# Kernel optimization log

Measured on AMD Instinct MI355X. Metric: run time of the kernel, lower is better.

The kernel has to match this reference:

```python
import jax, jax.numpy as jnp
import numpy as np

B, S, D = 4, 2048, 1024      # batch, seq, d_model
H = 4096                     # expert hidden_size
E, K = 8, 2                  # num_experts, top_k
Z_COEF, BAL_COEF = 0.001, 0.01


def setup_inputs() -> dict:
    key = jax.random.key(0)
    ks = jax.random.split(key, 10)
    sc = 0.02
    return {
        "x": jax.random.normal(ks[0], (B, S, D), jnp.float32),
        "gate_w": jax.random.normal(ks[1], (D, E), jnp.float32) * sc,
        "keys_w": jax.random.normal(ks[2], (E, D, H), jnp.float32) * sc,
        "keys_b": jnp.zeros((E, H), jnp.float32),
        "values_w": jax.random.normal(ks[3], (E, H, D), jnp.float32) * sc,
        "values_b": jnp.zeros((E, D), jnp.float32),
        "shared_keys_w": jax.random.normal(ks[4], (D, H), jnp.float32) * sc,
        "shared_keys_b": jnp.zeros((H,), jnp.float32),
        "shared_values_w": jax.random.normal(ks[5], (H, D), jnp.float32) * sc,
        "shared_values_b": jnp.zeros((D,), jnp.float32),
    }


def reference(x, gate_w, keys_w, keys_b, values_w, values_b,
              shared_keys_w, shared_keys_b, shared_values_w, shared_values_b):
    b, s, d = x.shape
    xf = x.reshape(-1, d)                                  # [N, D]

    # ---- Router (top-k, softmax over selected scores) ----
    logits = xf @ gate_w                                   # [N, E]
    scores, idx = jax.lax.top_k(logits, K)                 # [N, K]
    w = jax.nn.softmax(scores, axis=-1)                    # [N, K]

    # Aux losses (training path)
    one_hot = jax.nn.one_hot(idx, E, dtype=w.dtype)        # [N, K, E]
    usage = (one_hot * w[..., None]).sum(axis=(0, 1))      # [E]
    balance_loss = usage.std() / usage.mean() * BAL_COEF
    z_loss = jnp.square(jax.nn.logsumexp(logits, axis=-1)).mean() * Z_COEF
    router_loss = balance_loss + z_loss

    # ---- Shared expert(s): single FFN, divided by count (=1) ----
    out = jax.nn.gelu(xf @ shared_keys_w + shared_keys_b) @ shared_values_w + shared_values_b

    # ---- Training path: dense per-expert FFN, masked combine ----
    # hidden: [N, E, H]
    hidden = jax.nn.gelu(jnp.einsum('nd,edh->neh', xf, keys_w) + keys_b)
    expert_out = jnp.einsum('neh,ehd->ned', hidden, values_w) + values_b  # [N, E, D]
    comb = (one_hot * w[..., None]).sum(axis=1)            # [N, E] per-token expert weight
    out = out + jnp.einsum('ned,ne->nd', expert_out, comb)

    return out.reshape(b, s, d), router_loss
```

## Files before the change

kernel.cpp:

```cpp
#include <hip/hip_runtime.h>
#include <hip/hip_bf16.h>


#define N_TOK 8192
#define DM    1024
#define HD    4096
#define NE    8
#define NKTOT 16384
#define PERM_CAP 17408
#define MAX_TILES 136
#define BAND 17
#define EV_BLOCKS 1088
#define RTOK_BLK 16

typedef __attribute__((ext_vector_type(8))) short bhalf8;
typedef __attribute__((ext_vector_type(8))) unsigned short ushort8v;
typedef __attribute__((ext_vector_type(4))) float floatx4;

__device__ __forceinline__ unsigned short f2bf(float f) {
  union { float f; unsigned int u; } v; v.f = f;
  unsigned int u = v.u;
  return (unsigned short)((u + 0x7fffu + ((u >> 16) & 1u)) >> 16);
}

__device__ __forceinline__ float bf2f(unsigned short h) {
  union { unsigned int u; float f; } v; v.u = ((unsigned int)h) << 16;
  return v.f;
}

__device__ __forceinline__ float gelu_tanh(float h) {
  float u = 0.7978845608028654f * (h + 0.044715f * h * h * h);
  float t = 1.0f - 2.0f / (1.0f + __expf(2.0f * u));
  return 0.5f * h * (1.0f + t);
}

__device__ __forceinline__ void gload16(const unsigned short* g, void* l) {
  __builtin_amdgcn_global_load_lds(
      (const __attribute__((address_space(1))) void*)g,
      (__attribute__((address_space(3))) void*)l, 16, 0, 0);
}

__global__ void init_kernel(int* perm, float* permw, float* usage, float* zsum,
                            int* counts, int* fill) {
  int i = blockIdx.x * 256 + threadIdx.x;
  if (i < PERM_CAP) { perm[i] = 0; permw[i] = 0.0f; }
  if (i < NE) { usage[i] = 0.0f; counts[i] = 0; fill[i] = 0; }
  if (i == 0) zsum[0] = 0.0f;
}

__global__ void cvt_x_kernel(const float* __restrict__ x, unsigned short* __restrict__ xb) {
  size_t i = (size_t)(blockIdx.x * 256 + threadIdx.x) * 4;
  float4 v = *(const float4*)(x + i);
  ushort4 o;
  o.x = f2bf(v.x); o.y = f2bf(v.y); o.z = f2bf(v.z); o.w = f2bf(v.w);
  *(ushort4*)(xb + i) = o;
}

__global__ void router_kernel(const float* __restrict__ x, const float* __restrict__ gw,
                              int* __restrict__ idxb, float* __restrict__ wbuf,
                              float* __restrict__ usage, float* __restrict__ zsum,
                              int* __restrict__ counts) {
  __shared__ float s_use[NE];
  __shared__ int   s_cnt[NE];
  __shared__ float s_z;
  int t = threadIdx.x;
  if (t < NE) { s_use[t] = 0.0f; s_cnt[t] = 0; }
  if (t == 0) s_z = 0.0f;
  __syncthreads();

  int wave = t >> 6;
  int lane = t & 63;

  float luse[NE]; int lcnt[NE];
#pragma unroll
  for (int e = 0; e < NE; e++) { luse[e] = 0.0f; lcnt[e] = 0; }
  float lz = 0.0f;

#pragma unroll
  for (int i = 0; i < 4; i++) {
    int n = blockIdx.x * RTOK_BLK + wave * 4 + i;
    const float* xr = x + (size_t)n * DM;
    float acc[NE];
#pragma unroll
    for (int e = 0; e < NE; e++) acc[e] = 0.0f;
    for (int d = lane; d < DM; d += 64) {
      float xv = xr[d];
      const float* g = gw + (size_t)d * NE;
#pragma unroll
      for (int e = 0; e < NE; e++) acc[e] += xv * g[e];
    }
#pragma unroll
    for (int e = 0; e < NE; e++) {
#pragma unroll
      for (int off = 32; off > 0; off >>= 1) acc[e] += __shfl_xor(acc[e], off);
    }
    if (lane == 0) {
      float m1 = acc[0]; int i1 = 0;
#pragma unroll
      for (int e = 1; e < NE; e++) if (acc[e] > m1) { m1 = acc[e]; i1 = e; }
      float m2 = -3.0e38f; int i2 = 0;
#pragma unroll
      for (int e = 0; e < NE; e++) if (e != i1 && acc[e] > m2) { m2 = acc[e]; i2 = e; }
      float e1 = __expf(m2 - m1);
      float w1 = 1.0f / (1.0f + e1);
      float w2 = e1 / (1.0f + e1);
      float s = 0.0f;
#pragma unroll
      for (int e = 0; e < NE; e++) s += __expf(acc[e] - m1);
      float lse = m1 + __logf(s);
      idxb[n * 2 + 0] = i1; idxb[n * 2 + 1] = i2;
      wbuf[n * 2 + 0] = w1; wbuf[n * 2 + 1] = w2;
      luse[i1] += w1; luse[i2] += w2;
      lcnt[i1]++;     lcnt[i2]++;
      lz += lse * lse;
    }
  }

  if (lane == 0) {
#pragma unroll
    for (int e = 0; e < NE; e++) {
      atomicAdd(&s_use[e], luse[e]);
      atomicAdd(&s_cnt[e], lcnt[e]);
    }
    atomicAdd(&s_z, lz);
  }
  __syncthreads();
  if (t < NE) {
    atomicAdd(&usage[t], s_use[t]);
    atomicAdd(&counts[t], s_cnt[t]);
  }
  if (t == 0) atomicAdd(zsum, s_z);
}

__global__ void scan_kernel(const int* __restrict__ counts, int* __restrict__ poff,
                            int* __restrict__ tileE, int* __restrict__ tileR,
                            int* __restrict__ nTiles,
                            const float* __restrict__ usage, const float* __restrict__ zsum,
                            float* __restrict__ lossOut) {
  if (threadIdx.x == 0 && blockIdx.x == 0) {
    int run = 0, nt = 0;
    for (int e = 0; e < NE; e++) {
      poff[e] = run;
      int t = (counts[e] + 127) >> 7;
      for (int i = 0; i < t; i++) { tileE[nt] = e; tileR[nt] = run + i * 128; nt++; }
      run += t << 7;
    }
    *nTiles = nt;
    float mean = 0.0f;
    for (int e = 0; e < NE; e++) mean += usage[e];
    mean *= (1.0f / NE);
    float var = 0.0f;
    for (int e = 0; e < NE; e++) { float d = usage[e] - mean; var += d * d; }
    var *= (1.0f / NE);
    float bal = sqrtf(var) / mean * 0.01f;
    float z = (zsum[0] / (float)N_TOK) * 0.001f;
    lossOut[0] = bal + z;
  }
}

__global__ void scatter_kernel(const int* __restrict__ idxb, const float* __restrict__ wbuf,
                               const int* __restrict__ poff, int* __restrict__ fill,
                               int* __restrict__ perm, float* __restrict__ permw,
                               int* __restrict__ pos) {
  __shared__ int lcnt[NE];
  __shared__ int lbase[NE];
  int t = threadIdx.x;
  if (t < NE) lcnt[t] = 0;
  __syncthreads();
  int i = blockIdx.x * 256 + t;
  int e = idxb[i];
  int r = atomicAdd(&lcnt[e], 1);
  __syncthreads();
  if (t < NE) lbase[t] = atomicAdd(&fill[t], lcnt[t]);
  __syncthreads();
  int p = poff[e] + lbase[e] + r;
  perm[p] = i >> 1;
  permw[p] = wbuf[i];
  pos[i] = p;
}

__global__ void transpose_cvt_kernel(const float* __restrict__ src,
                                     unsigned short* __restrict__ dst, int R, int C) {
  __shared__ float tile[64][65];
  size_t bo = (size_t)blockIdx.z * R * C;
  src += bo; dst += bo;
  int r0 = blockIdx.x * 64, c0 = blockIdx.y * 64;
  int c = threadIdx.x & 63, r = threadIdx.x >> 6;
#pragma unroll
  for (int i = 0; i < 16; i++)
    tile[r + i * 4][c] = src[(size_t)(r0 + r + i * 4) * C + c0 + c];
  __syncthreads();
  int u = threadIdx.x & 7;
  int ow = threadIdx.x >> 3;
#pragma unroll
  for (int it = 0; it < 2; it++) {
    int oc = ow + it * 32;
    ushort8v o;
#pragma unroll
    for (int j = 0; j < 8; j++) o[j] = f2bf(tile[u * 8 + j][oc]);
    *(ushort8v*)&dst[(size_t)(c0 + oc) * R + r0 + u * 8] = o;
  }
}

__global__ void combine_kernel(float* __restrict__ out,
                               const unsigned short* __restrict__ eout,
                               const int* __restrict__ pos) {
  int t = blockIdx.x;
  int d = threadIdx.x * 8;
  int p0 = pos[t * 2], p1 = pos[t * 2 + 1];
  float* o = out + (size_t)t * DM + d;
  const unsigned short* e0 = eout + (size_t)p0 * DM + d;
  const unsigned short* e1 = eout + (size_t)p1 * DM + d;
  float4 a = *(const float4*)(o);
  float4 b = *(const float4*)(o + 4);
  ushort4 u0a = *(const ushort4*)(e0), u0b = *(const ushort4*)(e0 + 4);
  ushort4 u1a = *(const ushort4*)(e1), u1b = *(const ushort4*)(e1 + 4);
  a.x += bf2f(u0a.x) + bf2f(u1a.x);
  a.y += bf2f(u0a.y) + bf2f(u1a.y);
  a.z += bf2f(u0a.z) + bf2f(u1a.z);
  a.w += bf2f(u0a.w) + bf2f(u1a.w);
  b.x += bf2f(u0b.x) + bf2f(u1b.x);
  b.y += bf2f(u0b.y) + bf2f(u1b.y);
  b.z += bf2f(u0b.z) + bf2f(u1b.z);
  b.w += bf2f(u0b.w) + bf2f(u1b.w);
  *(float4*)(o) = a;
  *(float4*)(o + 4) = b;
}

template<int MODE>
__device__ __forceinline__ void gemm_body(
    int id,
    const unsigned short* __restrict__ A,
    const unsigned short* __restrict__ BT,
    const float* __restrict__ bias,
    float* __restrict__ outF,
    unsigned short* __restrict__ outH,
    int Kd, int Nd,
    const int* __restrict__ perm,
    const int* __restrict__ tileE,
    const int* __restrict__ tileR,
    const int* __restrict__ nTiles) {
  __shared__ __align__(16) unsigned short As[128 * 64];
  __shared__ __align__(16) unsigned short Bs[128 * 64];

  int xcd = id & 7, q = id >> 3;
  int mt, ntile;
  if (MODE == 1) {
    ntile = q & 7;
    mt = xcd * 8 + (q >> 3);
  } else {
    int n_in = q & 7, m_in = (q >> 3) & 3, ng = (q >> 5) & 3, mg = q >> 7;
    int mband = mg * 4 + m_in;
    if (mband >= BAND) return;
    mt = xcd * BAND + mband;
    ntile = ng * 8 + n_in;
  }

  int n0 = ntile * 128;
  int prow0 = 0, m0 = 0;
  if (MODE == 2) {
    if (mt >= *nTiles) return;
    int e = tileE[mt];
    prow0 = tileR[mt];
    BT += (size_t)e * Kd * Nd;
    bias += (size_t)e * Nd;
  } else {
    m0 = mt * 128;
  }

  int t = threadIdx.x;
  int rsub = t >> 3;
  int gc = (t & 7) ^ (rsub & 7);
  const unsigned short* aptr[4];
  const unsigned short* bptr[4];
#pragma unroll
  for (int p = 0; p < 4; p++) {
    int r = rsub + p * 32;
    size_t grow;
    if (MODE == 2) grow = (size_t)perm[prow0 + r];
    else           grow = (size_t)(m0 + r);
    aptr[p] = A + grow * Kd + gc * 8;
    bptr[p] = BT + (size_t)(n0 + r) * Kd + gc * 8;
  }
  char* ldsA = (char*)As + (t & 192) * 16;
  char* ldsB = (char*)Bs + (t & 192) * 16;

  int lane = t & 63;
  int wv = t >> 6;
  int wm = (wv >> 1) * 64, wn = (wv & 1) * 64;
  int lr = lane & 15, lq = lane >> 4;
  int rx = lr & 7;

  floatx4 acc[4][4];
#pragma unroll
  for (int i = 0; i < 4; i++)
#pragma unroll
    for (int j = 0; j < 4; j++) acc[i][j] = (floatx4){0.f, 0.f, 0.f, 0.f};

  for (int k0 = 0; k0 < Kd; k0 += 64) {
#pragma unroll
    for (int p = 0; p < 4; p++) {
      gload16(aptr[p] + k0, ldsA + p * 4096);
      gload16(bptr[p] + k0, ldsB + p * 4096);
    }
    __syncthreads();
#pragma unroll
    for (int kk = 0; kk < 2; kk++) {
      int ca = kk * 4 + lq;
      bhalf8 af[4], bf[4];
#pragma unroll
      for (int i = 0; i < 4; i++) {
        af[i] = *(const bhalf8*)&As[(wm + i * 16 + lr) * 64 + ((ca ^ rx) * 8)];
        bf[i] = *(const bhalf8*)&Bs[(wn + i * 16 + lr) * 64 + ((ca ^ rx) * 8)];
      }
#pragma unroll
      for (int mtile = 0; mtile < 4; mtile++)
#pragma unroll
        for (int ntl = 0; ntl < 4; ntl++)
          acc[mtile][ntl] = __builtin_amdgcn_mfma_f32_16x16x32_bf16(af[mtile], bf[ntl], acc[mtile][ntl], 0, 0, 0);
    }
    __syncthreads();
  }

#pragma unroll
  for (int mtile = 0; mtile < 4; mtile++) {
#pragma unroll
    for (int ntl = 0; ntl < 4; ntl++) {
      int ncol = n0 + wn + ntl * 16 + lr;
      float bb = bias[ncol];
#pragma unroll
      for (int r = 0; r < 4; r++) {
        int mrow = wm + mtile * 16 + lq * 4 + r;
        float v = acc[mtile][ntl][r] + bb;
        if (MODE == 1) {
          outF[(size_t)(m0 + mrow) * Nd + ncol] = v;
        } else {
          outH[(size_t)(prow0 + mrow) * Nd + ncol] = f2bf(gelu_tanh(v));
        }
      }
    }
  }
}

__global__ __launch_bounds__(256, 4) void gemm_expert_keys(
    const unsigned short* A, const unsigned short* BT, const float* bias,
    float* outF, unsigned short* outH, int Kd, int Nd,
    const int* perm, const int* tE, const int* tR, const int* nT) {
  gemm_body<2>(blockIdx.x, A, BT, bias, outF, outH, Kd, Nd, perm, tE, tR, nT);
}
__global__ __launch_bounds__(256, 4) void gemm_shared_values(
    const unsigned short* A, const unsigned short* BT, const float* bias,
    float* outF, unsigned short* outH, int Kd, int Nd,
    const int* perm, const int* tE, const int* tR, const int* nT) {
  gemm_body<1>(blockIdx.x, A, BT, bias, outF, outH, Kd, Nd, perm, tE, tR, nT);
}

__global__ __launch_bounds__(256, 4) void gemm_ev_sk(
    const unsigned short* __restrict__ hid, const unsigned short* __restrict__ wtV,
    const float* __restrict__ values_b, unsigned short* __restrict__ eout,
    const unsigned short* __restrict__ xb, const unsigned short* __restrict__ wtK8,
    const float* __restrict__ sk_b, unsigned short* __restrict__ hidS,
    const float* __restrict__ permw,
    const int* __restrict__ tileE, const int* __restrict__ tileR,
    const int* __restrict__ nTiles) {
  __shared__ __align__(16) unsigned short As[128 * 64];
  __shared__ __align__(16) unsigned short Bs[128 * 64];

  int id = blockIdx.x;
  bool is_ev = id < EV_BLOCKS;

  int Kd, rbase, n0;
  const unsigned short* A;
  const unsigned short* BT;
  const float* bias;
  if (is_ev) {
    int xcd = id & 7, q = id >> 3;
    int mt = xcd * BAND + (q >> 3);
    if (mt >= *nTiles) return;
    int e = tileE[mt];
    rbase = tileR[mt];
    n0 = (q & 7) * 128;
    Kd = HD;
    A = hid;
    BT = wtV + (size_t)e * HD * DM;
    bias = values_b + (size_t)e * DM;
  } else {
    int id2 = id - EV_BLOCKS;
    int xcd = id2 & 7, q = id2 >> 3;
    int mt = xcd * 8 + (q & 7);
    rbase = mt * 128;
    n0 = (q >> 3) * 128;
    Kd = DM;
    A = xb;
    BT = wtK8;
    bias = sk_b;
  }

  int t = threadIdx.x;
  int rsub = t >> 3;
  int gc = (t & 7) ^ (rsub & 7);
  const unsigned short* aptr[4];
  const unsigned short* bptr[4];
#pragma unroll
  for (int p = 0; p < 4; p++) {
    int r = rsub + p * 32;
    aptr[p] = A + (size_t)(rbase + r) * Kd + gc * 8;
    bptr[p] = BT + (size_t)(n0 + r) * Kd + gc * 8;
  }
  char* ldsA = (char*)As + (t & 192) * 16;
  char* ldsB = (char*)Bs + (t & 192) * 16;

  int lane = t & 63;
  int wv = t >> 6;
  int wm = (wv >> 1) * 64, wn = (wv & 1) * 64;
  int lr = lane & 15, lq = lane >> 4;
  int rx = lr & 7;

  floatx4 acc[4][4];
#pragma unroll
  for (int i = 0; i < 4; i++)
#pragma unroll
    for (int j = 0; j < 4; j++) acc[i][j] = (floatx4){0.f, 0.f, 0.f, 0.f};

  for (int k0 = 0; k0 < Kd; k0 += 64) {
#pragma unroll
    for (int p = 0; p < 4; p++) {
      gload16(aptr[p] + k0, ldsA + p * 4096);
      gload16(bptr[p] + k0, ldsB + p * 4096);
    }
    __syncthreads();
#pragma unroll
    for (int kk = 0; kk < 2; kk++) {
      int ca = kk * 4 + lq;
      bhalf8 af[4], bf[4];
#pragma unroll
      for (int i = 0; i < 4; i++) {
        af[i] = *(const bhalf8*)&As[(wm + i * 16 + lr) * 64 + ((ca ^ rx) * 8)];
        bf[i] = *(const bhalf8*)&Bs[(wn + i * 16 + lr) * 64 + ((ca ^ rx) * 8)];
      }
#pragma unroll
      for (int mtile = 0; mtile < 4; mtile++)
#pragma unroll
        for (int ntl = 0; ntl < 4; ntl++)
          acc[mtile][ntl] = __builtin_amdgcn_mfma_f32_16x16x32_bf16(af[mtile], bf[ntl], acc[mtile][ntl], 0, 0, 0);
    }
    __syncthreads();
  }

  if (is_ev) {
#pragma unroll
    for (int mtile = 0; mtile < 4; mtile++) {
#pragma unroll
      for (int ntl = 0; ntl < 4; ntl++) {
        int ncol = n0 + wn + ntl * 16 + lr;
        float bb = bias[ncol];
#pragma unroll
        for (int r = 0; r < 4; r++) {
          int prow = rbase + wm + mtile * 16 + lq * 4 + r;
          float w = permw[prow];
          float v = acc[mtile][ntl][r] + bb;
          eout[(size_t)prow * DM + ncol] = f2bf(w * v);
        }
      }
    }
  } else {
#pragma unroll
    for (int mtile = 0; mtile < 4; mtile++) {
#pragma unroll
      for (int ntl = 0; ntl < 4; ntl++) {
        int ncol = n0 + wn + ntl * 16 + lr;
        float bb = bias[ncol];
#pragma unroll
        for (int r = 0; r < 4; r++) {
          int mrow = rbase + wm + mtile * 16 + lq * 4 + r;
          float v = acc[mtile][ntl][r] + bb;
          hidS[(size_t)mrow * HD + ncol] = f2bf(gelu_tanh(v));
        }
      }
    }
  }
}

extern "C" void kernel_launch(void* const* d_in, const int* in_sizes, int n_in,
                              void* d_out, int out_size, void* d_ws, size_t ws_size,
                              hipStream_t stream) {
  const float* x        = (const float*)d_in[0];
  const float* gate_w   = (const float*)d_in[1];
  const float* keys_w   = (const float*)d_in[2];
  const float* keys_b   = (const float*)d_in[3];
  const float* values_w = (const float*)d_in[4];
  const float* values_b = (const float*)d_in[5];
  const float* sk_w     = (const float*)d_in[6];
  const float* sk_b     = (const float*)d_in[7];
  const float* sv_w     = (const float*)d_in[8];
  const float* sv_b     = (const float*)d_in[9];
  float* out = (float*)d_out;

  char* p = (char*)d_ws;
  unsigned short* xb   = (unsigned short*)p; p += (size_t)N_TOK * DM * 2;
  unsigned short* wt   = (unsigned short*)p; p += (size_t)(NE + 1) * DM * HD * 2;
  unsigned short* hid  = (unsigned short*)p; p += (size_t)(PERM_CAP + N_TOK) * HD * 2;
  unsigned short* eout = (unsigned short*)p; p += (size_t)PERM_CAP * DM * 2;
  int*   idxb   = (int*)p;   p += NKTOT * 4;
  float* wbuf   = (float*)p; p += NKTOT * 4;
  int*   perm   = (int*)p;   p += PERM_CAP * 4;
  float* permw  = (float*)p; p += PERM_CAP * 4;
  int*   pos    = (int*)p;   p += NKTOT * 4;
  int*   counts = (int*)p;   p += NE * 4;
  int*   fill   = (int*)p;   p += NE * 4;
  int*   poff   = (int*)p;   p += NE * 4;
  float* usage  = (float*)p; p += NE * 4;
  float* zsum   = (float*)p; p += 16;
  int*   tileE  = (int*)p;   p += MAX_TILES * 4;
  int*   tileR  = (int*)p;   p += MAX_TILES * 4;
  int*   nTiles = (int*)p;   p += 16;

  float* lossOut = out + (size_t)N_TOK * DM;
  unsigned short* wt8  = wt + (size_t)NE * DM * HD;
  unsigned short* hidS = hid + (size_t)PERM_CAP * HD;

  init_kernel<<<(PERM_CAP + 255) / 256, 256, 0, stream>>>(perm, permw, usage, zsum, counts, fill);
  cvt_x_kernel<<<(N_TOK * DM / 4 + 255) / 256, 256, 0, stream>>>(x, xb);
  router_kernel<<<N_TOK / RTOK_BLK, 256, 0, stream>>>(x, gate_w, idxb, wbuf, usage, zsum, counts);
  scan_kernel<<<1, 64, 0, stream>>>(counts, poff, tileE, tileR, nTiles, usage, zsum, lossOut);
  scatter_kernel<<<NKTOT / 256, 256, 0, stream>>>(idxb, wbuf, poff, fill, perm, permw, pos);

  transpose_cvt_kernel<<<dim3(DM / 64, HD / 64, NE), 256, 0, stream>>>(keys_w, wt, DM, HD);
  transpose_cvt_kernel<<<dim3(DM / 64, HD / 64, 1), 256, 0, stream>>>(sk_w, wt8, DM, HD);

  gemm_expert_keys<<<5120, 256, 0, stream>>>(
      xb, wt, keys_b, nullptr, hid, DM, HD, perm, tileE, tileR, nTiles);

  transpose_cvt_kernel<<<dim3(HD / 64, DM / 64, NE), 256, 0, stream>>>(values_w, wt, HD, DM);
  gemm_ev_sk<<<EV_BLOCKS + 2048, 256, 0, stream>>>(
      hid, wt, values_b, eout, xb, wt8, sk_b, hidS,
      permw, tileE, tileR, nTiles);

  transpose_cvt_kernel<<<dim3(HD / 64, DM / 64, 1), 256, 0, stream>>>(sv_w, wt8, HD, DM);
  gemm_shared_values<<<512, 256, 0, stream>>>(
      hidS, wt8, sv_b, out, nullptr, HD, DM, perm, tileE, tileR, nTiles);

  combine_kernel<<<N_TOK, 128, 0, stream>>>(out, eout, pos);
}
```

Before: 886.8 us.

## Fuse small kernels: cvt into router, atomics to per-block partials, combine into GEMM

```diff
diff --git a/kernel.cpp b/kernel.cpp
--- a/kernel.cpp
+++ b/kernel.cpp
@@ -12,6 +12,7 @@
 #define BAND 17
 #define EV_BLOCKS 1088
 #define RTOK_BLK 16
+#define NRB (N_TOK / RTOK_BLK)
 
 typedef __attribute__((ext_vector_type(8))) short bhalf8;
 typedef __attribute__((ext_vector_type(8))) unsigned short ushort8v;
@@ -40,26 +41,11 @@
       (__attribute__((address_space(3))) void*)l, 16, 0, 0);
 }
 
-__global__ void init_kernel(int* perm, float* permw, float* usage, float* zsum,
-                            int* counts, int* fill) {
-  int i = blockIdx.x * 256 + threadIdx.x;
-  if (i < PERM_CAP) { perm[i] = 0; permw[i] = 0.0f; }
-  if (i < NE) { usage[i] = 0.0f; counts[i] = 0; fill[i] = 0; }
-  if (i == 0) zsum[0] = 0.0f;
-}
-
-__global__ void cvt_x_kernel(const float* __restrict__ x, unsigned short* __restrict__ xb) {
-  size_t i = (size_t)(blockIdx.x * 256 + threadIdx.x) * 4;
-  float4 v = *(const float4*)(x + i);
-  ushort4 o;
-  o.x = f2bf(v.x); o.y = f2bf(v.y); o.z = f2bf(v.z); o.w = f2bf(v.w);
-  *(ushort4*)(xb + i) = o;
-}
-
 __global__ void router_kernel(const float* __restrict__ x, const float* __restrict__ gw,
                               int* __restrict__ idxb, float* __restrict__ wbuf,
-                              float* __restrict__ usage, float* __restrict__ zsum,
-                              int* __restrict__ counts) {
+                              unsigned short* __restrict__ xb,
+                              float* __restrict__ pb_use, int* __restrict__ pb_cnt,
+                              float* __restrict__ pb_z) {
   __shared__ float s_use[NE];
   __shared__ int   s_cnt[NE];
   __shared__ float s_z;
@@ -80,11 +66,13 @@
   for (int i = 0; i < 4; i++) {
     int n = blockIdx.x * RTOK_BLK + wave * 4 + i;
     const float* xr = x + (size_t)n * DM;
+    unsigned short* xbr = xb + (size_t)n * DM;
     float acc[NE];
 #pragma unroll
     for (int e = 0; e < NE; e++) acc[e] = 0.0f;
     for (int d = lane; d < DM; d += 64) {
       float xv = xr[d];
+      xbr[d] = f2bf(xv);
       const float* g = gw + (size_t)d * NE;
 #pragma unroll
       for (int e = 0; e < NE; e++) acc[e] += xv * g[e];
@@ -125,37 +113,61 @@
     atomicAdd(&s_z, lz);
   }
   __syncthreads();
+  int b = blockIdx.x;
+  if (t < NE) { pb_use[b * NE + t] = s_use[t]; pb_cnt[b * NE + t] = s_cnt[t]; }
+  if (t == 0) pb_z[b] = s_z;
+}
+
+__global__ void scan_kernel(const float* __restrict__ pb_use, const int* __restrict__ pb_cnt,
+                            const float* __restrict__ pb_z,
+                            int* __restrict__ poff, int* __restrict__ tileE,
+                            int* __restrict__ tileR, int* __restrict__ nTiles,
+                            int* __restrict__ fill, int* __restrict__ perm,
+                            float* __restrict__ permw, float* __restrict__ lossOut) {
+  __shared__ float sh_use[NE];
+  __shared__ int   sh_cnt[NE];
+  __shared__ float sh_z;
+  __shared__ int   sh_ps[NE], sh_pe[NE];
+  int t = threadIdx.x;
   if (t < NE) {
-    atomicAdd(&usage[t], s_use[t]);
-    atomicAdd(&counts[t], s_cnt[t]);
-  }
-  if (t == 0) atomicAdd(zsum, s_z);
-}
-
-__global__ void scan_kernel(const int* __restrict__ counts, int* __restrict__ poff,
-                            int* __restrict__ tileE, int* __restrict__ tileR,
-                            int* __restrict__ nTiles,
-                            const float* __restrict__ usage, const float* __restrict__ zsum,
-                            float* __restrict__ lossOut) {
-  if (threadIdx.x == 0 && blockIdx.x == 0) {
+    float s = 0.0f;
+    for (int b = 0; b < NRB; b++) s += pb_use[b * NE + t];
+    sh_use[t] = s;
+  } else if (t < 2 * NE) {
+    int e = t - NE; int s = 0;
+    for (int b = 0; b < NRB; b++) s += pb_cnt[b * NE + e];
+    sh_cnt[e] = s;
+  } else if (t == 2 * NE) {
+    float s = 0.0f;
+    for (int b = 0; b < NRB; b++) s += pb_z[b];
+    sh_z = s;
+  }
+  __syncthreads();
+  if (t == 0) {
     int run = 0, nt = 0;
     for (int e = 0; e < NE; e++) {
       poff[e] = run;
-      int t = (counts[e] + 127) >> 7;
-      for (int i = 0; i < t; i++) { tileE[nt] = e; tileR[nt] = run + i * 128; nt++; }
-      run += t << 7;
+      fill[e] = 0;
+      int tl = (sh_cnt[e] + 127) >> 7;
+      sh_ps[e] = run + sh_cnt[e];
+      sh_pe[e] = run + (tl << 7);
+      for (int i = 0; i < tl; i++) { tileE[nt] = e; tileR[nt] = run + i * 128; nt++; }
+      run += tl << 7;
     }
     *nTiles = nt;
     float mean = 0.0f;
-    for (int e = 0; e < NE; e++) mean += usage[e];
+    for (int e = 0; e < NE; e++) mean += sh_use[e];
     mean *= (1.0f / NE);
     float var = 0.0f;
-    for (int e = 0; e < NE; e++) { float d = usage[e] - mean; var += d * d; }
+    for (int e = 0; e < NE; e++) { float d = sh_use[e] - mean; var += d * d; }
     var *= (1.0f / NE);
     float bal = sqrtf(var) / mean * 0.01f;
-    float z = (zsum[0] / (float)N_TOK) * 0.001f;
+    float z = (sh_z / (float)N_TOK) * 0.001f;
     lossOut[0] = bal + z;
   }
+  __syncthreads();
+  for (int e = 0; e < NE; e++)
+    for (int i = sh_ps[e] + t; i < sh_pe[e]; i += 64) { perm[i] = 0; permw[i] = 0.0f; }
 }
 
 __global__ void scatter_kernel(const int* __restrict__ idxb, const float* __restrict__ wbuf,
@@ -179,11 +191,9 @@
   pos[i] = p;
 }
 
-__global__ void transpose_cvt_kernel(const float* __restrict__ src,
-                                     unsigned short* __restrict__ dst, int R, int C) {
+__device__ __forceinline__ void tr_body(const float* __restrict__ src,
+                                        unsigned short* __restrict__ dst, int R, int C) {
   __shared__ float tile[64][65];
-  size_t bo = (size_t)blockIdx.z * R * C;
-  src += bo; dst += bo;
   int r0 = blockIdx.x * 64, c0 = blockIdx.y * 64;
   int c = threadIdx.x & 63, r = threadIdx.x >> 6;
 #pragma unroll
@@ -202,157 +212,20 @@
   }
 }
 
-__global__ void combine_kernel(float* __restrict__ out,
-                               const unsigned short* __restrict__ eout,
-                               const int* __restrict__ pos) {
-  int t = blockIdx.x;
-  int d = threadIdx.x * 8;
-  int p0 = pos[t * 2], p1 = pos[t * 2 + 1];
-  float* o = out + (size_t)t * DM + d;
-  const unsigned short* e0 = eout + (size_t)p0 * DM + d;
-  const unsigned short* e1 = eout + (size_t)p1 * DM + d;
-  float4 a = *(const float4*)(o);
-  float4 b = *(const float4*)(o + 4);
-  ushort4 u0a = *(const ushort4*)(e0), u0b = *(const ushort4*)(e0 + 4);
-  ushort4 u1a = *(const ushort4*)(e1), u1b = *(const ushort4*)(e1 + 4);
-  a.x += bf2f(u0a.x) + bf2f(u1a.x);
-  a.y += bf2f(u0a.y) + bf2f(u1a.y);
-  a.z += bf2f(u0a.z) + bf2f(u1a.z);
-  a.w += bf2f(u0a.w) + bf2f(u1a.w);
-  b.x += bf2f(u0b.x) + bf2f(u1b.x);
-  b.y += bf2f(u0b.y) + bf2f(u1b.y);
-  b.z += bf2f(u0b.z) + bf2f(u1b.z);
-  b.w += bf2f(u0b.w) + bf2f(u1b.w);
-  *(float4*)(o) = a;
-  *(float4*)(o + 4) = b;
-}
-
-template<int MODE>
-__device__ __forceinline__ void gemm_body(
-    int id,
-    const unsigned short* __restrict__ A,
-    const unsigned short* __restrict__ BT,
-    const float* __restrict__ bias,
-    float* __restrict__ outF,
-    unsigned short* __restrict__ outH,
-    int Kd, int Nd,
-    const int* __restrict__ perm,
-    const int* __restrict__ tileE,
-    const int* __restrict__ tileR,
-    const int* __restrict__ nTiles) {
-  __shared__ __align__(16) unsigned short As[128 * 64];
-  __shared__ __align__(16) unsigned short Bs[128 * 64];
-
-  int xcd = id & 7, q = id >> 3;
-  int mt, ntile;
-  if (MODE == 1) {
-    ntile = q & 7;
-    mt = xcd * 8 + (q >> 3);
-  } else {
-    int n_in = q & 7, m_in = (q >> 3) & 3, ng = (q >> 5) & 3, mg = q >> 7;
-    int mband = mg * 4 + m_in;
-    if (mband >= BAND) return;
-    mt = xcd * BAND + mband;
-    ntile = ng * 8 + n_in;
-  }
-
-  int n0 = ntile * 128;
-  int prow0 = 0, m0 = 0;
-  if (MODE == 2) {
-    if (mt >= *nTiles) return;
-    int e = tileE[mt];
-    prow0 = tileR[mt];
-    BT += (size_t)e * Kd * Nd;
-    bias += (size_t)e * Nd;
-  } else {
-    m0 = mt * 128;
-  }
-
-  int t = threadIdx.x;
-  int rsub = t >> 3;
-  int gc = (t & 7) ^ (rsub & 7);
-  const unsigned short* aptr[4];
-  const unsigned short* bptr[4];
-#pragma unroll
-  for (int p = 0; p < 4; p++) {
-    int r = rsub + p * 32;
-    size_t grow;
-    if (MODE == 2) grow = (size_t)perm[prow0 + r];
-    else           grow = (size_t)(m0 + r);
-    aptr[p] = A + grow * Kd + gc * 8;
-    bptr[p] = BT + (size_t)(n0 + r) * Kd + gc * 8;
-  }
-  char* ldsA = (char*)As + (t & 192) * 16;
-  char* ldsB = (char*)Bs + (t & 192) * 16;
-
-  int lane = t & 63;
-  int wv = t >> 6;
-  int wm = (wv >> 1) * 64, wn = (wv & 1) * 64;
-  int lr = lane & 15, lq = lane >> 4;
-  int rx = lr & 7;
-
-  floatx4 acc[4][4];
-#pragma unroll
-  for (int i = 0; i < 4; i++)
-#pragma unroll
-    for (int j = 0; j < 4; j++) acc[i][j] = (floatx4){0.f, 0.f, 0.f, 0.f};
-
-  for (int k0 = 0; k0 < Kd; k0 += 64) {
-#pragma unroll
-    for (int p = 0; p < 4; p++) {
-      gload16(aptr[p] + k0, ldsA + p * 4096);
-      gload16(bptr[p] + k0, ldsB + p * 4096);
-    }
-    __syncthreads();
-#pragma unroll
-    for (int kk = 0; kk < 2; kk++) {
-      int ca = kk * 4 + lq;
-      bhalf8 af[4], bf[4];
-#pragma unroll
-      for (int i = 0; i < 4; i++) {
-        af[i] = *(const bhalf8*)&As[(wm + i * 16 + lr) * 64 + ((ca ^ rx) * 8)];
-        bf[i] = *(const bhalf8*)&Bs[(wn + i * 16 + lr) * 64 + ((ca ^ rx) * 8)];
-      }
-#pragma unroll
-      for (int mtile = 0; mtile < 4; mtile++)
-#pragma unroll
-        for (int ntl = 0; ntl < 4; ntl++)
-          acc[mtile][ntl] = __builtin_amdgcn_mfma_f32_16x16x32_bf16(af[mtile], bf[ntl], acc[mtile][ntl], 0, 0, 0);
-    }
-    __syncthreads();
-  }
-
-#pragma unroll
-  for (int mtile = 0; mtile < 4; mtile++) {
-#pragma unroll
-    for (int ntl = 0; ntl < 4; ntl++) {
-      int ncol = n0 + wn + ntl * 16 + lr;
-      float bb = bias[ncol];
-#pragma unroll
-      for (int r = 0; r < 4; r++) {
-        int mrow = wm + mtile * 16 + lq * 4 + r;
-        float v = acc[mtile][ntl][r] + bb;
-        if (MODE == 1) {
-          outF[(size_t)(m0 + mrow) * Nd + ncol] = v;
-        } else {
-          outH[(size_t)(prow0 + mrow) * Nd + ncol] = f2bf(gelu_tanh(v));
-        }
-      }
-    }
-  }
-}
-
-__global__ __launch_bounds__(256, 4) void gemm_expert_keys(
-    const unsigned short* A, const unsigned short* BT, const float* bias,
-    float* outF, unsigned short* outH, int Kd, int Nd,
-    const int* perm, const int* tE, const int* tR, const int* nT) {
-  gemm_body<2>(blockIdx.x, A, BT, bias, outF, outH, Kd, Nd, perm, tE, tR, nT);
-}
-__global__ __launch_bounds__(256, 4) void gemm_shared_values(
-    const unsigned short* A, const unsigned short* BT, const float* bias,
-    float* outF, unsigned short* outH, int Kd, int Nd,
-    const int* perm, const int* tE, const int* tR, const int* nT) {
-  gemm_body<1>(blockIdx.x, A, BT, bias, outF, outH, Kd, Nd, perm, tE, tR, nT);
+__global__ void transpose_cvt_kernel(const float* __restrict__ src,
+                                     unsigned short* __restrict__ dst, int R, int C) {
+  size_t bo = (size_t)blockIdx.z * R * C;
+  tr_body(src + bo, dst + bo, R, C);
+}
+
+__global__ void transpose_cvt9_kernel(const float* __restrict__ srcB,
+                                      const float* __restrict__ src1,
+                                      unsigned short* __restrict__ dstB,
+                                      unsigned short* __restrict__ dst1, int R, int C) {
+  int z = blockIdx.z;
+  const float* src = (z < NE) ? srcB + (size_t)z * R * C : src1;
+  unsigned short* dst = (z < NE) ? dstB + (size_t)z * R * C : dst1;
+  tr_body(src, dst, R, C);
 }
 
 __global__ __launch_bounds__(256, 4) void gemm_ev_sk(
@@ -481,6 +354,178 @@
   }
 }
 
+__global__ __launch_bounds__(256, 4) void gemm_expert_keys(
+    const unsigned short* __restrict__ A, const unsigned short* __restrict__ BT,
+    const float* __restrict__ bias, unsigned short* __restrict__ outH,
+    const int* __restrict__ perm, const int* __restrict__ tileE,
+    const int* __restrict__ tileR, const int* __restrict__ nTiles) {
+  __shared__ __align__(16) unsigned short As[128 * 64];
+  __shared__ __align__(16) unsigned short Bs[128 * 64];
+
+  int id = blockIdx.x;
+  int xcd = id & 7, q = id >> 3;
+  int n_in = q & 7, m_in = (q >> 3) & 3, ng = (q >> 5) & 3, mg = q >> 7;
+  int mband = mg * 4 + m_in;
+  if (mband >= BAND) return;
+  int mt = xcd * BAND + mband;
+  int ntile = ng * 8 + n_in;
+  if (mt >= *nTiles) return;
+  int e = tileE[mt];
+  int prow0 = tileR[mt];
+  const unsigned short* BTe = BT + (size_t)e * DM * HD;
+  const float* be = bias + (size_t)e * HD;
+  int n0 = ntile * 128;
+
+  int t = threadIdx.x;
+  int rsub = t >> 3;
+  int gc = (t & 7) ^ (rsub & 7);
+  const unsigned short* aptr[4];
+  const unsigned short* bptr[4];
+#pragma unroll
+  for (int p = 0; p < 4; p++) {
+    int r = rsub + p * 32;
+    aptr[p] = A + (size_t)perm[prow0 + r] * DM + gc * 8;
+    bptr[p] = BTe + (size_t)(n0 + r) * DM + gc * 8;
+  }
+  char* ldsA = (char*)As + (t & 192) * 16;
+  char* ldsB = (char*)Bs + (t & 192) * 16;
+
+  int lane = t & 63;
+  int wv = t >> 6;
+  int wm = (wv >> 1) * 64, wn = (wv & 1) * 64;
+  int lr = lane & 15, lq = lane >> 4;
+  int rx = lr & 7;
+
+  floatx4 acc[4][4];
+#pragma unroll
+  for (int i = 0; i < 4; i++)
+#pragma unroll
+    for (int j = 0; j < 4; j++) acc[i][j] = (floatx4){0.f, 0.f, 0.f, 0.f};
+
+  for (int k0 = 0; k0 < DM; k0 += 64) {
+#pragma unroll
+    for (int p = 0; p < 4; p++) {
+      gload16(aptr[p] + k0, ldsA + p * 4096);
+      gload16(bptr[p] + k0, ldsB + p * 4096);
+    }
+    __syncthreads();
+#pragma unroll
+    for (int kk = 0; kk < 2; kk++) {
+      int ca = kk * 4 + lq;
+      bhalf8 af[4], bf[4];
+#pragma unroll
+      for (int i = 0; i < 4; i++) {
+        af[i] = *(const bhalf8*)&As[(wm + i * 16 + lr) * 64 + ((ca ^ rx) * 8)];
+        bf[i] = *(const bhalf8*)&Bs[(wn + i * 16 + lr) * 64 + ((ca ^ rx) * 8)];
+      }
+#pragma unroll
+      for (int mtile = 0; mtile < 4; mtile++)
+#pragma unroll
+        for (int ntl = 0; ntl < 4; ntl++)
+          acc[mtile][ntl] = __builtin_amdgcn_mfma_f32_16x16x32_bf16(af[mtile], bf[ntl], acc[mtile][ntl], 0, 0, 0);
+    }
+    __syncthreads();
+  }
+
+#pragma unroll
+  for (int mtile = 0; mtile < 4; mtile++) {
+#pragma unroll
+    for (int ntl = 0; ntl < 4; ntl++) {
+      int ncol = n0 + wn + ntl * 16 + lr;
+      float bb = be[ncol];
+#pragma unroll
+      for (int r = 0; r < 4; r++) {
+        int mrow = wm + mtile * 16 + lq * 4 + r;
+        float v = acc[mtile][ntl][r] + bb;
+        outH[(size_t)(prow0 + mrow) * HD + ncol] = f2bf(gelu_tanh(v));
+      }
+    }
+  }
+}
+
+__global__ __launch_bounds__(256, 4) void gemm_sv_combine(
+    const unsigned short* __restrict__ A, const unsigned short* __restrict__ BT,
+    const float* __restrict__ bias, float* __restrict__ outF,
+    const unsigned short* __restrict__ eout, const int* __restrict__ pos) {
+  __shared__ __align__(16) unsigned short As[128 * 64];
+  __shared__ __align__(16) unsigned short Bs[128 * 64];
+
+  int id = blockIdx.x;
+  int xcd = id & 7, q = id >> 3;
+  int ntile = q & 7;
+  int mt = xcd * 8 + (q >> 3);
+  int n0 = ntile * 128, m0 = mt * 128;
+
+  int t = threadIdx.x;
+  int rsub = t >> 3;
+  int gc = (t & 7) ^ (rsub & 7);
+  const unsigned short* aptr[4];
+  const unsigned short* bptr[4];
+#pragma unroll
+  for (int p = 0; p < 4; p++) {
+    int r = rsub + p * 32;
+    aptr[p] = A + (size_t)(m0 + r) * HD + gc * 8;
+    bptr[p] = BT + (size_t)(n0 + r) * HD + gc * 8;
+  }
+  char* ldsA = (char*)As + (t & 192) * 16;
+  char* ldsB = (char*)Bs + (t & 192) * 16;
+
+  int lane = t & 63;
+  int wv = t >> 6;
+  int wm = (wv >> 1) * 64, wn = (wv & 1) * 64;
+  int lr = lane & 15, lq = lane >> 4;
+  int rx = lr & 7;
+
+  floatx4 acc[4][4];
+#pragma unroll
+  for (int i = 0; i < 4; i++)
+#pragma unroll
+    for (int j = 0; j < 4; j++) acc[i][j] = (floatx4){0.f, 0.f, 0.f, 0.f};
+
+  for (int k0 = 0; k0 < HD; k0 += 64) {
+#pragma unroll
+    for (int p = 0; p < 4; p++) {
+      gload16(aptr[p] + k0, ldsA + p * 4096);
+      gload16(bptr[p] + k0, ldsB + p * 4096);
+    }
+    __syncthreads();
+#pragma unroll
+    for (int kk = 0; kk < 2; kk++) {
+      int ca = kk * 4 + lq;
+      bhalf8 af[4], bf[4];
+#pragma unroll
+      for (int i = 0; i < 4; i++) {
+        af[i] = *(const bhalf8*)&As[(wm + i * 16 + lr) * 64 + ((ca ^ rx) * 8)];
+        bf[i] = *(const bhalf8*)&Bs[(wn + i * 16 + lr) * 64 + ((ca ^ rx) * 8)];
+      }
+#pragma unroll
+      for (int mtile = 0; mtile < 4; mtile++)
+#pragma unroll
+        for (int ntl = 0; ntl < 4; ntl++)
+          acc[mtile][ntl] = __builtin_amdgcn_mfma_f32_16x16x32_bf16(af[mtile], bf[ntl], acc[mtile][ntl], 0, 0, 0);
+    }
+    __syncthreads();
+  }
+
+#pragma unroll
+  for (int mtile = 0; mtile < 4; mtile++) {
+#pragma unroll
+    for (int ntl = 0; ntl < 4; ntl++) {
+      int ncol = n0 + wn + ntl * 16 + lr;
+      float bb = bias[ncol];
+#pragma unroll
+      for (int r = 0; r < 4; r++) {
+        int mrow = m0 + wm + mtile * 16 + lq * 4 + r;
+        int p0 = pos[mrow * 2], p1 = pos[mrow * 2 + 1];
+        float v = acc[mtile][ntl][r] + bb
+                + bf2f(eout[(size_t)p0 * DM + ncol])
+                + bf2f(eout[(size_t)p1 * DM + ncol]);
+        outF[(size_t)mrow * DM + ncol] = v;
+      }
+    }
+  }
+}
+
 extern "C" void kernel_launch(void* const* d_in, const int* in_sizes, int n_in,
                               void* d_out, int out_size, void* d_ws, size_t ws_size,
                               hipStream_t stream) {
@@ -506,11 +551,11 @@
   int*   perm   = (int*)p;   p += PERM_CAP * 4;
   float* permw  = (float*)p; p += PERM_CAP * 4;
   int*   pos    = (int*)p;   p += NKTOT * 4;
-  int*   counts = (int*)p;   p += NE * 4;
+  float* pb_use = (float*)p; p += NRB * NE * 4;
+  int*   pb_cnt = (int*)p;   p += NRB * NE * 4;
+  float* pb_z   = (float*)p; p += NRB * 4;
   int*   fill   = (int*)p;   p += NE * 4;
   int*   poff   = (int*)p;   p += NE * 4;
-  float* usage  = (float*)p; p += NE * 4;
-  float* zsum   = (float*)p; p += 16;
   int*   tileE  = (int*)p;   p += MAX_TILES * 4;
   int*   tileR  = (int*)p;   p += MAX_TILES * 4;
   int*   nTiles = (int*)p;   p += 16;
@@ -519,17 +564,16 @@
   unsigned short* wt8  = wt + (size_t)NE * DM * HD;
   unsigned short* hidS = hid + (size_t)PERM_CAP * HD;
 
-  init_kernel<<<(PERM_CAP + 255) / 256, 256, 0, stream>>>(perm, permw, usage, zsum, counts, fill);
-  cvt_x_kernel<<<(N_TOK * DM / 4 + 255) / 256, 256, 0, stream>>>(x, xb);
-  router_kernel<<<N_TOK / RTOK_BLK, 256, 0, stream>>>(x, gate_w, idxb, wbuf, usage, zsum, counts);
-  scan_kernel<<<1, 64, 0, stream>>>(counts, poff, tileE, tileR, nTiles, usage, zsum, lossOut);
+  router_kernel<<<NRB, 256, 0, stream>>>(x, gate_w, idxb, wbuf, xb, pb_use, pb_cnt, pb_z);
+  scan_kernel<<<1, 64, 0, stream>>>(pb_use, pb_cnt, pb_z, poff, tileE, tileR, nTiles,
+                                    fill, perm, permw, lossOut);
   scatter_kernel<<<NKTOT / 256, 256, 0, stream>>>(idxb, wbuf, poff, fill, perm, permw, pos);
 
-  transpose_cvt_kernel<<<dim3(DM / 64, HD / 64, NE), 256, 0, stream>>>(keys_w, wt, DM, HD);
-  transpose_cvt_kernel<<<dim3(DM / 64, HD / 64, 1), 256, 0, stream>>>(sk_w, wt8, DM, HD);
+  transpose_cvt9_kernel<<<dim3(DM / 64, HD / 64, NE + 1), 256, 0, stream>>>(
+      keys_w, sk_w, wt, wt8, DM, HD);
 
   gemm_expert_keys<<<5120, 256, 0, stream>>>(
-      xb, wt, keys_b, nullptr, hid, DM, HD, perm, tileE, tileR, nTiles);
+      xb, wt, keys_b, hid, perm, tileE, tileR, nTiles);
 
   transpose_cvt_kernel<<<dim3(HD / 64, DM / 64, NE), 256, 0, stream>>>(values_w, wt, HD, DM);
   gemm_ev_sk<<<EV_BLOCKS + 2048, 256, 0, stream>>>(
@@ -537,8 +581,6 @@
       permw, tileE, tileR, nTiles);
 
   transpose_cvt_kernel<<<dim3(HD / 64, DM / 64, 1), 256, 0, stream>>>(sv_w, wt8, HD, DM);
-  gemm_shared_values<<<512, 256, 0, stream>>>(
-      hidS, wt8, sv_b, out, nullptr, HD, DM, perm, tileE, tileR, nTiles);
-
-  combine_kernel<<<N_TOK, 128, 0, stream>>>(out, eout, pos);
-}
+  gemm_sv_combine<<<512, 256, 0, stream>>>(
+      hidS, wt8, sv_b, out, eout, pos);
+}
```

Measured after the change: 1.131 ms. +27.5%, slower.
